# Optimization experiments

Hardware: AMD Instinct MI355X
Metric: run time of the kernel (lower is better)

## Reference

```python
import jax, jax.numpy as jnp
import numpy as np

T, B, V, E = 256, 128, 256, 512
NN = (1024, 1024)  # num_nodes per LSTM layer


def setup_inputs() -> dict:
    key = jax.random.key(0)
    ks = jax.random.split(key, 8)
    inputs = jax.random.normal(ks[0], (T, B, V), jnp.float32)
    emb = jax.random.normal(ks[1], (V, E), jnp.float32) * np.float32(np.sqrt(1.0 / V))
    w0 = jax.random.normal(ks[2], (E + NN[0], 4 * NN[0]), jnp.float32) * np.float32(np.sqrt(1.0 / (E + NN[0])))
    b0 = jnp.zeros((4 * NN[0],), jnp.float32)
    w1 = jax.random.normal(ks[3], (NN[0] + NN[1], 4 * NN[1]), jnp.float32) * np.float32(np.sqrt(1.0 / (NN[0] + NN[1])))
    b1 = jnp.zeros((4 * NN[1],), jnp.float32)
    out_w = jax.random.normal(ks[4], (NN[1], V), jnp.float32) * np.float32(np.sqrt(1.0 / NN[1]))
    out_b = jnp.zeros((V,), jnp.float32)
    return {"inputs": inputs, "embedding_matrix": emb,
            "lstm_w0": w0, "lstm_b0": b0, "lstm_w1": w1, "lstm_b1": b1,
            "out_w": out_w, "out_b": out_b}


def reference(inputs, embedding_matrix, lstm_w0, lstm_b0, lstm_w1, lstm_b1, out_w, out_b):
    Tn, Bn, _ = inputs.shape
    # _embed: (stacked one-hot) @ embedding_matrix -> [T, B, E]
    embs = jnp.einsum('tbv,ve->tbe', inputs, embedding_matrix)
    ws = (lstm_w0, lstm_w1)
    bs = (lstm_b0, lstm_b1)
    init_states = tuple((jnp.zeros((Bn, n), embs.dtype), jnp.zeros((Bn, n), embs.dtype)) for n in NN)

    def step(states, emb):
        out = emb
        new_states = []
        for i in range(len(NN)):
            h, c = states[i]
            n = NN[i]
            # concat([dropout(inp), h]) @ W + b ; dropout_keep_prob = 1.0 -> identity
            lin = jnp.concatenate([out, h], axis=1) @ ws[i] + bs[i]
            f = jax.nn.sigmoid(lin[:, :n])
            ig = jax.nn.sigmoid(lin[:, n:2 * n])
            o = jax.nn.sigmoid(lin[:, 2 * n:3 * n])
            g = jnp.tanh(lin[:, 3 * n:])
            c = f * c + ig * g
            h = o * jnp.tanh(c)
            out = h
            new_states.append((h, c))
        return tuple(new_states), out

    _, rnn_outputs = jax.lax.scan(step, init_states, embs)  # [T, B, NN[-1]]
    # output module: concat over time (axis 0) then single dense layer
    hs = rnn_outputs.reshape(Tn * Bn, NN[-1])
    logits = hs @ out_w + out_b  # [T*B, V]
    return logits
```

## Files before the change

kernel.cpp:

```cpp
#include <hip/hip_runtime.h>
#include <hip/hip_bf16.h>
#include <cstdint>
#include <cstddef>

#define T_STEPS 256
#define BATCH   128
#define VOCAB   256
#define EDIM    512
#define NH      1024
#define GDIM    4096
#define NST0    40
#define NST1    64

typedef __attribute__((ext_vector_type(8))) short short8;
typedef __attribute__((ext_vector_type(4))) float floatx4;

__device__ __forceinline__ float sigmoidf_(float x) { return 1.0f / (1.0f + __expf(-x)); }
__device__ __forceinline__ float tanhf_(float x)    { return 1.0f - 2.0f / (__expf(2.0f * x) + 1.0f); }

typedef __attribute__((address_space(1))) const unsigned int guint;
typedef __attribute__((address_space(3))) unsigned int luint;
__device__ __forceinline__ void load_lds16(const void* g, void* l) {
    __builtin_amdgcn_global_load_lds((guint*)g, (luint*)l, 16, 0, 0);
}

#define BM 128
#define BN 128
#define BK 16
__global__ __launch_bounds__(256) void sgemm_f32(
    const float* __restrict__ A, const float* __restrict__ B,
    float* __restrict__ C, int M, int N, int K)
{
    __shared__ float As[BK][BM + 4];
    __shared__ float Bs[BK][BN + 4];
    const int tid = threadIdx.x;
    const int tr = tid >> 4, tc = tid & 15;
    const int bm = blockIdx.y, bn = blockIdx.x;
    const float* Ab = A + (size_t)bm * BM * K;
    float acc[8][8];
    #pragma unroll
    for (int i = 0; i < 8; ++i)
        #pragma unroll
        for (int j = 0; j < 8; ++j) acc[i][j] = 0.f;
    for (int k0 = 0; k0 < K; k0 += BK) {
        #pragma unroll
        for (int l = 0; l < 2; ++l) {
            int idx = tid + l * 256;
            int row = idx >> 2, c4 = idx & 3;
            float4 v = *(const float4*)(Ab + (size_t)row * K + k0 + c4 * 4);
            As[c4 * 4 + 0][row] = v.x; As[c4 * 4 + 1][row] = v.y;
            As[c4 * 4 + 2][row] = v.z; As[c4 * 4 + 3][row] = v.w;
        }
        #pragma unroll
        for (int l = 0; l < 2; ++l) {
            int idx = tid + l * 256;
            int row = idx >> 5, c4 = idx & 31;
            *(float4*)&Bs[row][c4 * 4] = *(const float4*)(B + (size_t)(k0 + row) * N + bn * BN + c4 * 4);
        }
        __syncthreads();
        #pragma unroll
        for (int kk = 0; kk < BK; ++kk) {
            float4 a0 = *(const float4*)&As[kk][tr * 8];
            float4 a1 = *(const float4*)&As[kk][tr * 8 + 4];
            float4 b0 = *(const float4*)&Bs[kk][tc * 8];
            float4 b1 = *(const float4*)&Bs[kk][tc * 8 + 4];
            float av[8] = {a0.x, a0.y, a0.z, a0.w, a1.x, a1.y, a1.z, a1.w};
            float bv[8] = {b0.x, b0.y, b0.z, b0.w, b1.x, b1.y, b1.z, b1.w};
            #pragma unroll
            for (int i = 0; i < 8; ++i)
                #pragma unroll
                for (int j = 0; j < 8; ++j) acc[i][j] += av[i] * bv[j];
        }
        __syncthreads();
    }
    #pragma unroll
    for (int i = 0; i < 8; ++i) {
        size_t row = (size_t)bm * BM + tr * 8 + i;
        #pragma unroll
        for (int j = 0; j < 8; j += 4) {
            int col = bn * BN + tc * 8 + j;
            *(float4*)(C + row * N + col) =
                make_float4(acc[i][j], acc[i][j+1], acc[i][j+2], acc[i][j+3]);
        }
    }
}

__global__ __launch_bounds__(256) void transpose_to_bf16(
    const float* __restrict__ src, __hip_bfloat16* __restrict__ dst, int R, int C)
{
    __shared__ float t[32][33];
    int x = blockIdx.x * 32 + threadIdx.x;
    #pragma unroll
    for (int i = 0; i < 4; ++i) {
        int y = blockIdx.y * 32 + threadIdx.y + i * 8;
        t[threadIdx.y + i * 8][threadIdx.x] = src[(size_t)y * C + x];
    }
    __syncthreads();
    int x2 = blockIdx.y * 32 + threadIdx.x;
    #pragma unroll
    for (int i = 0; i < 4; ++i) {
        int y2 = blockIdx.x * 32 + threadIdx.y + i * 8;
        dst[(size_t)y2 * R + x2] = __float2bfloat16(t[threadIdx.x][threadIdx.y + i * 8]);
    }
}

__global__ __launch_bounds__(256) void pack_w2(
    const float* __restrict__ src, __hip_bfloat16* __restrict__ dst,
    int koff, int NSTEPS)
{
    __shared__ float t[64][33];
    const int tid = threadIdx.x;
    const int xt = blockIdx.x;
    const int kt = blockIdx.y;
    {
        int yl = tid >> 3;
        int x0 = (tid & 7) * 8;
        const float* p = src + (size_t)(kt * 32 + yl) * GDIM + xt * 64 + x0;
        float4 v0 = *(const float4*)p;
        float4 v1 = *(const float4*)(p + 4);
        t[x0 + 0][yl] = v0.x; t[x0 + 1][yl] = v0.y; t[x0 + 2][yl] = v0.z; t[x0 + 3][yl] = v0.w;
        t[x0 + 4][yl] = v1.x; t[x0 + 5][yl] = v1.y; t[x0 + 6][yl] = v1.z; t[x0 + 7][yl] = v1.w;
    }
    __syncthreads();
    {
        int ll = tid >> 2;
        int quad = tid & 3;
        int lincol = xt * 64 + ll;
        int g = lincol >> 10, n = lincol & 1023;
        int j = n >> 3, c = n & 7;
        int tt = g >> 1;
        int l16 = (g & 1) * 8 + c;
        int s = (koff >> 5) + kt;
        __hip_bfloat16 o[8];
        #pragma unroll
        for (int jj = 0; jj < 8; ++jj)
            o[jj] = __float2bfloat16(t[ll][quad * 8 + jj]);
        size_t off = ((((size_t)j * NSTEPS + s) * 2 + tt) * 64 + (size_t)quad * 16 + l16) * 8;
        *(uint4*)(dst + off) = *(const uint4*)o;
    }
}

__global__ __launch_bounds__(256) void convert_to_bf16(
    const float* __restrict__ src, __hip_bfloat16* __restrict__ dst, size_t n4)
{
    size_t i = (size_t)blockIdx.x * 256 + threadIdx.x;
    if (i < n4) {
        float4 v = *(const float4*)(src + i * 4);
        __hip_bfloat16 o[4] = {__float2bfloat16(v.x), __float2bfloat16(v.y),
                               __float2bfloat16(v.z), __float2bfloat16(v.w)};
        *(uint2*)(dst + i * 4) = *(uint2*)o;
    }
}

#define GKP 40
__global__ __launch_bounds__(256) void gemm_bt(
    const __hip_bfloat16* __restrict__ A, const __hip_bfloat16* __restrict__ Bt,
    const float* __restrict__ bias, float* __restrict__ C, int M, int N, int K)
{
    __shared__ __hip_bfloat16 As[128 * GKP];
    __shared__ __hip_bfloat16 Bs[128 * GKP];
    const int tid = threadIdx.x;
    const int wave = tid >> 6, lane = tid & 63;
    const int quad = lane >> 4, l16 = lane & 15;
    const int wm = (wave >> 1) * 64, wn = (wave & 1) * 64;
    const size_t Arow0 = (size_t)blockIdx.y * 128;
    const size_t Brow0 = (size_t)blockIdx.x * 128;
    floatx4 acc[4][4];
    #pragma unroll
    for (int i = 0; i < 4; ++i)
        #pragma unroll
        for (int j = 0; j < 4; ++j) acc[i][j] = (floatx4)0.f;

    for (int k0 = 0; k0 < K; k0 += 32) {
        #pragma unroll
        for (int l = 0; l < 2; ++l) {
            int idx = tid + l * 256;
            int row = idx >> 2, seg = idx & 3;
            *(uint4*)(As + row * GKP + seg * 8) =
                *(const uint4*)(A + (Arow0 + row) * K + k0 + seg * 8);
            *(uint4*)(Bs + row * GKP + seg * 8) =
                *(const uint4*)(Bt + (Brow0 + row) * K + k0 + seg * 8);
        }
        __syncthreads();
        short8 af[4], bf[4];
        #pragma unroll
        for (int i = 0; i < 4; ++i)
            af[i] = *(const short8*)(As + (wm + i * 16 + l16) * GKP + quad * 8);
        #pragma unroll
        for (int j = 0; j < 4; ++j)
            bf[j] = *(const short8*)(Bs + (wn + j * 16 + l16) * GKP + quad * 8);
        #pragma unroll
        for (int i = 0; i < 4; ++i)
            #pragma unroll
            for (int j = 0; j < 4; ++j)
                acc[i][j] = __builtin_amdgcn_mfma_f32_16x16x32_bf16(af[i], bf[j], acc[i][j], 0, 0, 0);
        __syncthreads();
    }
    #pragma unroll
    for (int i = 0; i < 4; ++i)
        #pragma unroll
        for (int j = 0; j < 4; ++j) {
            int col = (int)Brow0 + wn + j * 16 + l16;
            float bv = bias ? bias[col] : 0.f;
            #pragma unroll
            for (int r = 0; r < 4; ++r) {
                size_t row = Arow0 + wm + i * 16 + quad * 4 + r;
                C[row * N + col] = acc[i][j][r] + bv;
            }
        }
}

template<int NCF, int NCS, int WF, int WS>
__device__ __forceinline__ void chunks2(
    const __hip_bfloat16* __restrict__ pF,
    const __hip_bfloat16* __restrict__ pS,
    const __hip_bfloat16* Wlds, int lane,
    floatx4& acc0, floatx4& acc1)
{
    constexpr int NC = NCF + NCS;
    constexpr int D = (NC < 3) ? NC : 3;
    short8 af[3][8];
    #pragma unroll
    for (int c = 0; c < D; ++c) {
        const __hip_bfloat16* pa = (c < NCF) ? (pF + (size_t)c * 256)
                                             : (pS + (size_t)(c - NCF) * 256);
        #pragma unroll
        for (int ss = 0; ss < 8; ++ss)
            af[c % D][ss] = *(const short8*)(pa + ss * 32);
    }
    #pragma unroll
    for (int c = 0; c < NC; ++c) {
        const int wc = (c < NCF) ? (WF + c) : (WS + (c - NCF));
        #pragma unroll
        for (int ss = 0; ss < 8; ++ss) {
            const int s = wc * 8 + ss;
            short8 bf0 = *(const short8*)&Wlds[s * 1024 + lane * 8];
            short8 bf1 = *(const short8*)&Wlds[s * 1024 + 512 + lane * 8];
            acc0 = __builtin_amdgcn_mfma_f32_16x16x32_bf16(af[c % D][ss], bf0, acc0, 0, 0, 0);
            acc1 = __builtin_amdgcn_mfma_f32_16x16x32_bf16(af[c % D][ss], bf1, acc1, 0, 0, 0);
        }
        if (c + D < NC) {
            const int cn = c + D;
            const __hip_bfloat16* pa = (cn < NCF) ? (pF + (size_t)cn * 256)
                                                  : (pS + (size_t)(cn - NCF) * 256);
            #pragma unroll
            for (int ss = 0; ss < 8; ++ss)
                af[cn % D][ss] = *(const short8*)(pa + ss * 32);
        }
    }
}

__global__ __launch_bounds__(512) void lstm_diag(
    const __hip_bfloat16* __restrict__ inbf,
    const __hip_bfloat16* __restrict__ Wpack0,
    const __hip_bfloat16* __restrict__ Wpack1,
    const float* __restrict__ b0, const float* __restrict__ b1,
    __hip_bfloat16* __restrict__ h0_cur,
    const __hip_bfloat16* __restrict__ h0_prev,
    float* __restrict__ c0, float* __restrict__ c1,
    __hip_bfloat16* __restrict__ H1all,
    int d)
{
    const int bid = blockIdx.x;
    const int layer = (bid >> 3) & 1;
    const int j = ((bid >> 4) << 3) | (bid & 7);
    if (layer == 0 && d >= T_STEPS) return;
    if (layer == 1 && d == 0) return;

    __shared__ __attribute__((aligned(16))) __hip_bfloat16 Wlds[65536];

    const int tid = threadIdx.x;
    const int wave = tid >> 6, lane = tid & 63;
    const int quad = lane >> 4, l16 = lane & 15;

    const __hip_bfloat16 *A0, *A1;
    int A0stride;
    const float* bb; float* cst; __hip_bfloat16* hout;
    bool first;
    if (layer == 0) {
        first = (d == 0);
        bb = b0; cst = c0;
        A0 = inbf + (size_t)d * (BATCH * VOCAB); A0stride = VOCAB;
        A1 = h0_prev;
        hout = h0_cur;
        const __hip_bfloat16* Wp = Wpack0 + (size_t)j * (NST0 * 1024);
        #pragma unroll
        for (int it = 0; it < 10; ++it)
            load_lds16(Wp + it * 4096 + tid * 8, Wlds + it * 4096 + tid * 8);
    } else {
        first = (d == 1);
        bb = b1; cst = c1;
        A0 = h0_prev; A0stride = NH;
        A1 = (d >= 2) ? (H1all + (size_t)(d - 2) * (BATCH * NH)) : h0_prev;
        hout = H1all + (size_t)(d - 1) * (BATCH * NH);
        const __hip_bfloat16* Wp = Wpack1 + (size_t)j * (NST1 * 1024);
        #pragma unroll
        for (int it = 0; it < 16; ++it)
            load_lds16(Wp + it * 4096 + tid * 8, Wlds + it * 4096 + tid * 8);
    }

    const int row = wave * 16 + l16;
    const __hip_bfloat16* pA0 = A0 + (size_t)row * A0stride + quad * 8;
    const __hip_bfloat16* pA1 = A1 + (size_t)row * NH + quad * 8;

    const int cc = j * 8 + (l16 & 7);
    float bv0 = bb[((l16 < 8) ? 0 : 1) * NH + cc];
    float bv1 = bb[((l16 < 8) ? 2 : 3) * NH + cc];
    float cold[4];
    {
        const int bbase = 16 * wave + quad * 4;
        #pragma unroll
        for (int r = 0; r < 4; ++r)
            cold[r] = first ? 0.f : cst[(size_t)(bbase + r) * NH + cc];
    }
    floatx4 acc0 = {bv0, bv0, bv0, bv0};
    floatx4 acc1 = {bv1, bv1, bv1, bv1};

    __syncthreads();
    if (layer == 0) {
        if (first) chunks2<1, 0, 0, 0>(pA0, pA0, Wlds, lane, acc0, acc1);
        else       chunks2<1, 4, 0, 1>(pA0, pA1, Wlds, lane, acc0, acc1);
    } else {
        if (first) chunks2<4, 0, 0, 0>(pA0, pA0, Wlds, lane, acc0, acc1);
        else       chunks2<4, 4, 4, 0>(pA1, pA0, Wlds, lane, acc0, acc1);
    }

    #pragma unroll
    for (int r = 0; r < 4; ++r) {
        float a0 = acc0[r], a1 = acc1[r];
        float p0 = __shfl_xor(a0, 8, 64);
        float p1 = __shfl_xor(a1, 8, 64);
        if (l16 < 8) {
            int b = 16 * wave + quad * 4 + r;
            float f  = sigmoidf_(a0);
            float ig = sigmoidf_(p0);
            float oo = sigmoidf_(a1);
            float gg = tanhf_(p1);
            size_t idx = (size_t)b * NH + cc;
            float cn = f * cold[r] + ig * gg;
            float hn = oo * tanhf_(cn);
            cst[idx] = cn;
            hout[idx] = __float2bfloat16(hn);
        }
    }
}

__device__ __forceinline__ void grid_barrier_nf(uint32_t* cnt, uint32_t target) {
    __syncthreads();
    asm volatile("" ::: "memory");
    if (threadIdx.x == 0) {
        __hip_atomic_fetch_add(cnt, 1u, __ATOMIC_RELAXED, __HIP_MEMORY_SCOPE_AGENT);
        while (__hip_atomic_load(cnt, __ATOMIC_RELAXED, __HIP_MEMORY_SCOPE_AGENT) < target)
            __builtin_amdgcn_s_sleep(1);
    }
    __syncthreads();
    asm volatile("" ::: "memory");
}

__global__ void zero_u32(uint32_t* p) { *p = 0; }

__global__ __launch_bounds__(512) void lstm_persist3(
    const __hip_bfloat16* __restrict__ inbf,
    const __hip_bfloat16* __restrict__ Wpack0,
    const __hip_bfloat16* __restrict__ Wpack1,
    const float* __restrict__ b0, const float* __restrict__ b1,
    __hip_bfloat16* __restrict__ H0all,
    __hip_bfloat16* __restrict__ H1all,
    uint32_t* __restrict__ bar)
{
    __shared__ __attribute__((aligned(16))) __hip_bfloat16 Wlds[65536];

    const int bid = blockIdx.x;
    const int layer = (bid >> 3) & 1;
    const int j = ((bid >> 4) << 3) | (bid & 7);
    const int tid = threadIdx.x;
    const int wave = tid >> 6, lane = tid & 63;
    const int quad = lane >> 4, l16 = lane & 15;

    if (layer == 0) {
        const __hip_bfloat16* Wp = Wpack0 + (size_t)j * (NST0 * 1024);
        #pragma unroll
        for (int it = 0; it < 10; ++it)
            load_lds16(Wp + it * 4096 + tid * 8, Wlds + it * 4096 + tid * 8);
    } else {
        const __hip_bfloat16* Wp = Wpack1 + (size_t)j * (NST1 * 1024);
        #pragma unroll
        for (int it = 0; it < 16; ++it)
            load_lds16(Wp + it * 4096 + tid * 8, Wlds + it * 4096 + tid * 8);
    }
    __syncthreads();

    const int cc = j * 8 + (l16 & 7);
    const float* bb = layer ? b1 : b0;
    const float bv0 = bb[((l16 < 8) ? 0 : 1) * NH + cc];
    const float bv1 = bb[((l16 < 8) ? 2 : 3) * NH + cc];
    const int row = wave * 16 + l16;
    float creg[4] = {0.f, 0.f, 0.f, 0.f};

    for (int d = 0; d <= T_STEPS; ++d) {
        if (d) grid_barrier_nf(bar, (uint32_t)d * 256u);

        const bool active = layer ? (d >= 1) : (d < T_STEPS);
        if (!active) continue;

        const __hip_bfloat16 *A0, *A1;
        int A0stride;
        bool first;
        __hip_bfloat16* hout;
        if (layer == 0) {
            first = (d == 0);
            A0 = inbf + (size_t)d * (BATCH * VOCAB); A0stride = VOCAB;
            A1 = first ? H0all : (H0all + (size_t)(d - 1) * (BATCH * NH));
            hout = H0all + (size_t)d * (BATCH * NH);
        } else {
            first = (d == 1);
            A0 = H0all + (size_t)(d - 1) * (BATCH * NH); A0stride = NH;
            A1 = (d >= 2) ? (H1all + (size_t)(d - 2) * (BATCH * NH)) : A0;
            hout = H1all + (size_t)(d - 1) * (BATCH * NH);
        }

        const __hip_bfloat16* pA0 = A0 + (size_t)row * A0stride + quad * 8;
        const __hip_bfloat16* pA1 = A1 + (size_t)row * NH + quad * 8;
        floatx4 acc0 = {bv0, bv0, bv0, bv0};
        floatx4 acc1 = {bv1, bv1, bv1, bv1};

        if (layer == 0) {
            if (first) chunks2<1, 0, 0, 0>(pA0, pA0, Wlds, lane, acc0, acc1);
            else       chunks2<1, 4, 0, 1>(pA0, pA1, Wlds, lane, acc0, acc1);
        } else {
            if (first) chunks2<4, 0, 0, 0>(pA0, pA0, Wlds, lane, acc0, acc1);
            else       chunks2<4, 4, 4, 0>(pA1, pA0, Wlds, lane, acc0, acc1);
        }

        #pragma unroll
        for (int r = 0; r < 4; ++r) {
            float a0 = acc0[r], a1 = acc1[r];
            float p0 = __shfl_xor(a0, 8, 64);
            float p1 = __shfl_xor(a1, 8, 64);
            float f  = sigmoidf_(a0);
            float ig = sigmoidf_(p0);
            float oo = sigmoidf_(a1);
            float gg = tanhf_(p1);
            float cn = f * (first ? 0.f : creg[r]) + ig * gg;
            if (l16 < 8) creg[r] = cn;
            float hn = oo * tanhf_(cn);
            union { __hip_bfloat16 h; unsigned short u; } cv;
            cv.h = __float2bfloat16(hn);
            unsigned int other = __shfl_xor((unsigned int)cv.u, 1, 64);
            if (l16 < 8 && !(l16 & 1)) {
                unsigned int packed = (unsigned int)cv.u | (other << 16);
                int b = 16 * wave + quad * 4 + r;
                __hip_atomic_store((unsigned int*)&hout[(size_t)b * NH + cc],
                                   packed, __ATOMIC_RELAXED, __HIP_MEMORY_SCOPE_AGENT);
            }
        }
    }
}

extern "C" void kernel_launch(void* const* d_in, const int* in_sizes, int n_in,
                              void* d_out, int out_size, void* d_ws, size_t ws_size,
                              hipStream_t stream)
{
    const float* inputs = (const float*)d_in[0];
    const float* emb    = (const float*)d_in[1];
    const float* w0     = (const float*)d_in[2];
    const float* b0     = (const float*)d_in[3];
    const float* w1     = (const float*)d_in[4];
    const float* b1     = (const float*)d_in[5];
    const float* outw   = (const float*)d_in[6];
    const float* outb   = (const float*)d_in[7];
    float* out = (float*)d_out;

    char* ws = (char*)d_ws;
    size_t off = 0;
    auto take = [&](size_t bytes) { char* p = ws + off; off += (bytes + 255) & ~(size_t)255; return p; };
    float* Wcomb = (float*)take((size_t)VOCAB * GDIM * 4);
    __hip_bfloat16* Wpack0 = (__hip_bfloat16*)take((size_t)128 * NST0 * 1024 * 2);
    __hip_bfloat16* Wpack1 = (__hip_bfloat16*)take((size_t)128 * NST1 * 1024 * 2);
    __hip_bfloat16* outwt  = (__hip_bfloat16*)take((size_t)NH * VOCAB * 2);
    __hip_bfloat16* inbf   = (__hip_bfloat16*)take((size_t)T_STEPS * BATCH * VOCAB * 2);
    __hip_bfloat16* h0pp0  = (__hip_bfloat16*)take((size_t)BATCH * NH * 2);
    __hip_bfloat16* h0pp1  = (__hip_bfloat16*)take((size_t)BATCH * NH * 2);
    float* c0 = (float*)take((size_t)BATCH * NH * 4);
    float* c1 = (float*)take((size_t)BATCH * NH * 4);
    uint32_t* bar = (uint32_t*)take(256);
    __hip_bfloat16* H1all  = (__hip_bfloat16*)take((size_t)T_STEPS * BATCH * NH * 2);
    __hip_bfloat16* H0all  = (__hip_bfloat16*)take((size_t)T_STEPS * BATCH * NH * 2);
    const bool ws_ok = (off <= ws_size);

    sgemm_f32<<<dim3(GDIM / BN, VOCAB / BM), 256, 0, stream>>>(
        emb, w0, Wcomb, VOCAB, GDIM, EDIM);
    pack_w2<<<dim3(64, VOCAB / 32), 256, 0, stream>>>(Wcomb, Wpack0, 0, NST0);
    pack_w2<<<dim3(64, NH / 32), 256, 0, stream>>>(w0 + (size_t)EDIM * GDIM, Wpack0, VOCAB, NST0);
    pack_w2<<<dim3(64, NH / 32), 256, 0, stream>>>(w1, Wpack1, 0, NST1);
    pack_w2<<<dim3(64, NH / 32), 256, 0, stream>>>(w1 + (size_t)NH * GDIM, Wpack1, NH, NST1);
    transpose_to_bf16<<<dim3(VOCAB / 32, NH / 32), dim3(32, 8), 0, stream>>>(
        outw, outwt, NH, VOCAB);
    {
        size_t n4 = (size_t)T_STEPS * BATCH * VOCAB / 4;
        convert_to_bf16<<<(int)((n4 + 255) / 256), 256, 0, stream>>>(inputs, inbf, n4);
    }
    zero_u32<<<1, 1, 0, stream>>>(bar);

    bool done = false;
    if (ws_ok) {
        void* args[] = { (void*)&inbf, (void*)&Wpack0, (void*)&Wpack1,
                         (void*)&b0, (void*)&b1,
                         (void*)&H0all, (void*)&H1all, (void*)&bar };
        hipError_t ce = hipLaunchCooperativeKernel(lstm_persist3, dim3(256), dim3(512),
                                                   args, 0u, stream);
        done = (ce == hipSuccess);
    }
    if (!done) {
        for (int d = 0; d <= T_STEPS; ++d) {
            __hip_bfloat16* hcur = (d & 1) ? h0pp1 : h0pp0;
            __hip_bfloat16* hprev = (d & 1) ? h0pp0 : h0pp1;
            lstm_diag<<<256, 512, 0, stream>>>(
                inbf, Wpack0, Wpack1, b0, b1, hcur, hprev, c0, c1, H1all, d);
        }
    }

    gemm_bt<<<dim3(VOCAB / 128, (T_STEPS * BATCH) / 128), 256, 0, stream>>>(
        H1all, outwt, outb, out, T_STEPS * BATCH, VOCAB, NH);
}
```

Measured before the change: 5.804 ms.

## Replace global grid barrier with per-block epoch flags and layer decoupling

Each block now publishes a per-column epoch counter instead of joining a single atomic grid barrier. Layer-0 blocks wait only for all layer-0 producers of the previous step, and layer-1 blocks wait for the flags they actually depend on. Layer 1 can also prefetch its own recurrent state before waiting on layer 0, so the two layers pipeline instead of running in lockstep. The risk is extra polling traffic (64 lanes each poll two flags) and correctness depending on relaxed ordering of the h stores relative to the flag stores.

New measurement: 5.029 ms. -13.4%, faster.

```diff
diff --git a/kernel.cpp b/kernel.cpp
--- a/kernel.cpp
+++ b/kernel.cpp
@@ -210,24 +210,33 @@
         }
 }
 
+struct AfBuf { short8 a[3][8]; };
+
+template<int NCF, int NCS>
+__device__ __forceinline__ void chunks_pro(
+    AfBuf& B, const __hip_bfloat16* __restrict__ pF,
+    const __hip_bfloat16* __restrict__ pS)
+{
+    constexpr int NC = NCF + NCS;
+    constexpr int D = (NC < 3) ? NC : 3;
+    #pragma unroll
+    for (int c = 0; c < D; ++c) {
+        const __hip_bfloat16* pa = (c < NCF) ? (pF + (size_t)c * 256)
+                                             : (pS + (size_t)(c - NCF) * 256);
+        #pragma unroll
+        for (int ss = 0; ss < 8; ++ss)
+            B.a[c][ss] = *(const short8*)(pa + ss * 32);
+    }
+}
+
 template<int NCF, int NCS, int WF, int WS>
-__device__ __forceinline__ void chunks2(
-    const __hip_bfloat16* __restrict__ pF,
+__device__ __forceinline__ void chunks_main(
+    AfBuf& B, const __hip_bfloat16* __restrict__ pF,
     const __hip_bfloat16* __restrict__ pS,
     const __hip_bfloat16* Wlds, int lane,
     floatx4& acc0, floatx4& acc1)
 {
     constexpr int NC = NCF + NCS;
-    constexpr int D = (NC < 3) ? NC : 3;
-    short8 af[3][8];
-    #pragma unroll
-    for (int c = 0; c < D; ++c) {
-        const __hip_bfloat16* pa = (c < NCF) ? (pF + (size_t)c * 256)
-                                             : (pS + (size_t)(c - NCF) * 256);
-        #pragma unroll
-        for (int ss = 0; ss < 8; ++ss)
-            af[c % D][ss] = *(const short8*)(pa + ss * 32);
-    }
     #pragma unroll
     for (int c = 0; c < NC; ++c) {
         const int wc = (c < NCF) ? (WF + c) : (WS + (c - NCF));
@@ -236,16 +245,16 @@
             const int s = wc * 8 + ss;
             short8 bf0 = *(const short8*)&Wlds[s * 1024 + lane * 8];
             short8 bf1 = *(const short8*)&Wlds[s * 1024 + 512 + lane * 8];
-            acc0 = __builtin_amdgcn_mfma_f32_16x16x32_bf16(af[c % D][ss], bf0, acc0, 0, 0, 0);
-            acc1 = __builtin_amdgcn_mfma_f32_16x16x32_bf16(af[c % D][ss], bf1, acc1, 0, 0, 0);
-        }
-        if (c + D < NC) {
-            const int cn = c + D;
+            acc0 = __builtin_amdgcn_mfma_f32_16x16x32_bf16(B.a[c % 3][ss], bf0, acc0, 0, 0, 0);
+            acc1 = __builtin_amdgcn_mfma_f32_16x16x32_bf16(B.a[c % 3][ss], bf1, acc1, 0, 0, 0);
+        }
+        if (c + 3 < NC) {
+            const int cn = c + 3;
             const __hip_bfloat16* pa = (cn < NCF) ? (pF + (size_t)cn * 256)
                                                   : (pS + (size_t)(cn - NCF) * 256);
             #pragma unroll
             for (int ss = 0; ss < 8; ++ss)
-                af[cn % D][ss] = *(const short8*)(pa + ss * 32);
+                B.a[cn % 3][ss] = *(const short8*)(pa + ss * 32);
         }
     }
 }
@@ -316,13 +325,14 @@
     floatx4 acc0 = {bv0, bv0, bv0, bv0};
     floatx4 acc1 = {bv1, bv1, bv1, bv1};
 
+    AfBuf B;
     __syncthreads();
     if (layer == 0) {
-        if (first) chunks2<1, 0, 0, 0>(pA0, pA0, Wlds, lane, acc0, acc1);
-        else       chunks2<1, 4, 0, 1>(pA0, pA1, Wlds, lane, acc0, acc1);
+        if (first) { chunks_pro<1, 0>(B, pA0, pA0); chunks_main<1, 0, 0, 0>(B, pA0, pA0, Wlds, lane, acc0, acc1); }
+        else       { chunks_pro<1, 4>(B, pA0, pA1); chunks_main<1, 4, 0, 1>(B, pA0, pA1, Wlds, lane, acc0, acc1); }
     } else {
-        if (first) chunks2<4, 0, 0, 0>(pA0, pA0, Wlds, lane, acc0, acc1);
-        else       chunks2<4, 4, 4, 0>(pA1, pA0, Wlds, lane, acc0, acc1);
+        if (first) { chunks_pro<4, 0>(B, pA0, pA0); chunks_main<4, 0, 0, 0>(B, pA0, pA0, Wlds, lane, acc0, acc1); }
+        else       { chunks_pro<4, 4>(B, pA1, pA0); chunks_main<4, 4, 4, 0>(B, pA1, pA0, Wlds, lane, acc0, acc1); }
     }
 
     #pragma unroll
@@ -345,21 +355,31 @@
     }
 }
 
-__device__ __forceinline__ void grid_barrier_nf(uint32_t* cnt, uint32_t target) {
+__device__ __forceinline__ void spin_all_ge(const uint32_t* ep, uint32_t target,
+                                            int lane, int wave) {
+    asm volatile("" ::: "memory");
+    if (wave == 0) {
+        for (;;) {
+            uint32_t a = __hip_atomic_load(&ep[lane], __ATOMIC_RELAXED, __HIP_MEMORY_SCOPE_AGENT);
+            uint32_t b = __hip_atomic_load(&ep[lane + 64], __ATOMIC_RELAXED, __HIP_MEMORY_SCOPE_AGENT);
+            if (__all(a >= target && b >= target)) break;
+            __builtin_amdgcn_s_sleep(1);
+        }
+    }
+    __builtin_amdgcn_s_barrier();
+    asm volatile("" ::: "memory");
+}
+
+__device__ __forceinline__ void arrive_ep(uint32_t* slot, uint32_t val) {
     __syncthreads();
     asm volatile("" ::: "memory");
-    if (threadIdx.x == 0) {
-        __hip_atomic_fetch_add(cnt, 1u, __ATOMIC_RELAXED, __HIP_MEMORY_SCOPE_AGENT);
-        while (__hip_atomic_load(cnt, __ATOMIC_RELAXED, __HIP_MEMORY_SCOPE_AGENT) < target)
-            __builtin_amdgcn_s_sleep(1);
-    }
-    __syncthreads();
-    asm volatile("" ::: "memory");
-}
-
-__global__ void zero_u32(uint32_t* p) { *p = 0; }
-
-__global__ __launch_bounds__(512) void lstm_persist3(
+    if (threadIdx.x == 0)
+        __hip_atomic_store(slot, val, __ATOMIC_RELAXED, __HIP_MEMORY_SCOPE_AGENT);
+}
+
+__global__ void zero_bar(uint32_t* p) { p[threadIdx.x] = 0; }
+
+__global__ __launch_bounds__(512) void lstm_persist4(
     const __hip_bfloat16* __restrict__ inbf,
     const __hip_bfloat16* __restrict__ Wpack0,
     const __hip_bfloat16* __restrict__ Wpack1,
@@ -377,6 +397,9 @@
     const int wave = tid >> 6, lane = tid & 63;
     const int quad = lane >> 4, l16 = lane & 15;
 
+    uint32_t* ep0 = bar;
+    uint32_t* ep1 = bar + 128;
+
     if (layer == 0) {
         const __hip_bfloat16* Wp = Wpack0 + (size_t)j * (NST0 * 1024);
         #pragma unroll
@@ -397,62 +420,93 @@
     const int row = wave * 16 + l16;
     float creg[4] = {0.f, 0.f, 0.f, 0.f};
 
-    for (int d = 0; d <= T_STEPS; ++d) {
-        if (d) grid_barrier_nf(bar, (uint32_t)d * 256u);
-
-        const bool active = layer ? (d >= 1) : (d < T_STEPS);
-        if (!active) continue;
-
-        const __hip_bfloat16 *A0, *A1;
-        int A0stride;
-        bool first;
-        __hip_bfloat16* hout;
-        if (layer == 0) {
-            first = (d == 0);
-            A0 = inbf + (size_t)d * (BATCH * VOCAB); A0stride = VOCAB;
-            A1 = first ? H0all : (H0all + (size_t)(d - 1) * (BATCH * NH));
-            hout = H0all + (size_t)d * (BATCH * NH);
-        } else {
-            first = (d == 1);
-            A0 = H0all + (size_t)(d - 1) * (BATCH * NH); A0stride = NH;
-            A1 = (d >= 2) ? (H1all + (size_t)(d - 2) * (BATCH * NH)) : A0;
-            hout = H1all + (size_t)(d - 1) * (BATCH * NH);
-        }
-
-        const __hip_bfloat16* pA0 = A0 + (size_t)row * A0stride + quad * 8;
-        const __hip_bfloat16* pA1 = A1 + (size_t)row * NH + quad * 8;
-        floatx4 acc0 = {bv0, bv0, bv0, bv0};
-        floatx4 acc1 = {bv1, bv1, bv1, bv1};
-
-        if (layer == 0) {
-            if (first) chunks2<1, 0, 0, 0>(pA0, pA0, Wlds, lane, acc0, acc1);
-            else       chunks2<1, 4, 0, 1>(pA0, pA1, Wlds, lane, acc0, acc1);
-        } else {
-            if (first) chunks2<4, 0, 0, 0>(pA0, pA0, Wlds, lane, acc0, acc1);
-            else       chunks2<4, 4, 4, 0>(pA1, pA0, Wlds, lane, acc0, acc1);
-        }
-
-        #pragma unroll
-        for (int r = 0; r < 4; ++r) {
-            float a0 = acc0[r], a1 = acc1[r];
-            float p0 = __shfl_xor(a0, 8, 64);
-            float p1 = __shfl_xor(a1, 8, 64);
-            float f  = sigmoidf_(a0);
-            float ig = sigmoidf_(p0);
-            float oo = sigmoidf_(a1);
-            float gg = tanhf_(p1);
-            float cn = f * (first ? 0.f : creg[r]) + ig * gg;
-            if (l16 < 8) creg[r] = cn;
-            float hn = oo * tanhf_(cn);
-            union { __hip_bfloat16 h; unsigned short u; } cv;
-            cv.h = __float2bfloat16(hn);
-            unsigned int other = __shfl_xor((unsigned int)cv.u, 1, 64);
-            if (l16 < 8 && !(l16 & 1)) {
-                unsigned int packed = (unsigned int)cv.u | (other << 16);
-                int b = 16 * wave + quad * 4 + r;
-                __hip_atomic_store((unsigned int*)&hout[(size_t)b * NH + cc],
-                                   packed, __ATOMIC_RELAXED, __HIP_MEMORY_SCOPE_AGENT);
+    if (layer == 0) {
+        for (int d = 0; d < T_STEPS; ++d) {
+            const bool first = (d == 0);
+            const __hip_bfloat16* pA0 =
+                inbf + (size_t)d * (BATCH * VOCAB) + (size_t)row * VOCAB + quad * 8;
+            __hip_bfloat16* hout = H0all + (size_t)d * (BATCH * NH);
+            floatx4 acc0 = {bv0, bv0, bv0, bv0};
+            floatx4 acc1 = {bv1, bv1, bv1, bv1};
+            AfBuf B;
+            if (first) {
+                chunks_pro<1, 0>(B, pA0, pA0);
+                chunks_main<1, 0, 0, 0>(B, pA0, pA0, Wlds, lane, acc0, acc1);
+            } else {
+                spin_all_ge(ep0, (uint32_t)d, lane, wave);
+                const __hip_bfloat16* pA1 =
+                    H0all + (size_t)(d - 1) * (BATCH * NH) + (size_t)row * NH + quad * 8;
+                chunks_pro<1, 4>(B, pA0, pA1);
+                chunks_main<1, 4, 0, 1>(B, pA0, pA1, Wlds, lane, acc0, acc1);
             }
+            #pragma unroll
+            for (int r = 0; r < 4; ++r) {
+                float a0 = acc0[r], a1 = acc1[r];
+                float p0 = __shfl_xor(a0, 8, 64);
+                float p1 = __shfl_xor(a1, 8, 64);
+                float f  = sigmoidf_(a0);
+                float ig = sigmoidf_(p0);
+                float oo = sigmoidf_(a1);
+                float gg = tanhf_(p1);
+                float cn = f * (first ? 0.f : creg[r]) + ig * gg;
+                if (l16 < 8) creg[r] = cn;
+                float hn = oo * tanhf_(cn);
+                union { __hip_bfloat16 h; unsigned short u; } cv;
+                cv.h = __float2bfloat16(hn);
+                unsigned int other = __shfl_xor((unsigned int)cv.u, 1, 64);
+                if (l16 < 8 && !(l16 & 1)) {
+                    unsigned int packed = (unsigned int)cv.u | (other << 16);
+                    int b = 16 * wave + quad * 4 + r;
+                    __hip_atomic_store((unsigned int*)&hout[(size_t)b * NH + cc],
+                                       packed, __ATOMIC_RELAXED, __HIP_MEMORY_SCOPE_AGENT);
+                }
+            }
+            arrive_ep(&ep0[j], (uint32_t)(d + 1));
+        }
+    } else {
+        for (int d = 1; d <= T_STEPS; ++d) {
+            const bool first = (d == 1);
+            const __hip_bfloat16* pA0 =
+                H0all + (size_t)(d - 1) * (BATCH * NH) + (size_t)row * NH + quad * 8;
+            __hip_bfloat16* hout = H1all + (size_t)(d - 1) * (BATCH * NH);
+            floatx4 acc0 = {bv0, bv0, bv0, bv0};
+            floatx4 acc1 = {bv1, bv1, bv1, bv1};
+            AfBuf B;
+            if (first) {
+                spin_all_ge(ep0, 1u, lane, wave);
+                chunks_pro<4, 0>(B, pA0, pA0);
+                chunks_main<4, 0, 0, 0>(B, pA0, pA0, Wlds, lane, acc0, acc1);
+            } else {
+                spin_all_ge(ep1, (uint32_t)(d - 1), lane, wave);
+                const __hip_bfloat16* pA1 =
+                    H1all + (size_t)(d - 2) * (BATCH * NH) + (size_t)row * NH + quad * 8;
+                chunks_pro<4, 4>(B, pA1, pA0);
+                spin_all_ge(ep0, (uint32_t)d, lane, wave);
+                chunks_main<4, 4, 4, 0>(B, pA1, pA0, Wlds, lane, acc0, acc1);
+            }
+            #pragma unroll
+            for (int r = 0; r < 4; ++r) {
+                float a0 = acc0[r], a1 = acc1[r];
+                float p0 = __shfl_xor(a0, 8, 64);
+                float p1 = __shfl_xor(a1, 8, 64);
+                float f  = sigmoidf_(a0);
+                float ig = sigmoidf_(p0);
+                float oo = sigmoidf_(a1);
+                float gg = tanhf_(p1);
+                float cn = f * (first ? 0.f : creg[r]) + ig * gg;
+                if (l16 < 8) creg[r] = cn;
+                float hn = oo * tanhf_(cn);
+                union { __hip_bfloat16 h; unsigned short u; } cv;
+                cv.h = __float2bfloat16(hn);
+                unsigned int other = __shfl_xor((unsigned int)cv.u, 1, 64);
+                if (l16 < 8 && !(l16 & 1)) {
+                    unsigned int packed = (unsigned int)cv.u | (other << 16);
+                    int b = 16 * wave + quad * 4 + r;
+                    __hip_atomic_store((unsigned int*)&hout[(size_t)b * NH + cc],
+                                       packed, __ATOMIC_RELAXED, __HIP_MEMORY_SCOPE_AGENT);
+                }
+            }
+            arrive_ep(&ep1[j], (uint32_t)d);
         }
     }
 }
@@ -483,7 +537,7 @@
     __hip_bfloat16* h0pp1  = (__hip_bfloat16*)take((size_t)BATCH * NH * 2);
     float* c0 = (float*)take((size_t)BATCH * NH * 4);
     float* c1 = (float*)take((size_t)BATCH * NH * 4);
-    uint32_t* bar = (uint32_t*)take(256);
+    uint32_t* bar = (uint32_t*)take(1024);
     __hip_bfloat16* H1all  = (__hip_bfloat16*)take((size_t)T_STEPS * BATCH * NH * 2);
     __hip_bfloat16* H0all  = (__hip_bfloat16*)take((size_t)T_STEPS * BATCH * NH * 2);
     const bool ws_ok = (off <= ws_size);
@@ -500,14 +554,14 @@
         size_t n4 = (size_t)T_STEPS * BATCH * VOCAB / 4;
         convert_to_bf16<<<(int)((n4 + 255) / 256), 256, 0, stream>>>(inputs, inbf, n4);
     }
-    zero_u32<<<1, 1, 0, stream>>>(bar);
+    zero_bar<<<1, 256, 0, stream>>>(bar);
 
     bool done = false;
     if (ws_ok) {
         void* args[] = { (void*)&inbf, (void*)&Wpack0, (void*)&Wpack1,
                          (void*)&b0, (void*)&b1,
                          (void*)&H0all, (void*)&H1all, (void*)&bar };
-        hipError_t ce = hipLaunchCooperativeKernel(lstm_persist3, dim3(256), dim3(512),
+        hipError_t ce = hipLaunchCooperativeKernel(lstm_persist4, dim3(256), dim3(512),
                                                    args, 0u, stream);
         done = (ce == hipSuccess);
     }
```
